# Kernel optimization log

Hardware: AMD Instinct MI355X
Metric: run time of the kernel (lower is better)

The kernel has to match this reference:

```python
import jax, jax.numpy as jnp
import numpy as np

ALPHA = 0.2  # LeakyReLU negative slope
N, IN_DIM, OUT_DIM = 8192, 128, 64


def setup_inputs() -> dict:
    key = jax.random.key(0)
    k1, k2, k3, k4 = jax.random.split(key, 4)
    x = jax.random.normal(k1, (N, IN_DIM), dtype=jnp.float32)
    adj = jax.random.randint(k2, (N, N), 0, 2, dtype=jnp.int32)
    W = jax.random.normal(k3, (IN_DIM, OUT_DIM), dtype=jnp.float32) * 0.1
    a = jax.random.normal(k4, (2 * OUT_DIM, 1), dtype=jnp.float32) * 0.1
    return {"x": x, "adj": adj, "W": W, "a": a}


def reference(x, adj, W, a):
    # h = x @ W : [N, out]
    h = x @ W
    # e_ij = LeakyReLU(a^T [h_i || h_j]) computed as broadcast sum of the
    # two halves of the attention vector (avoids materializing [N,N,2*out]).
    a_src = a[:OUT_DIM, 0]   # [out]
    a_dst = a[OUT_DIM:, 0]   # [out]
    e = (h @ a_src)[:, None] + (h @ a_dst)[None, :]      # [N, N]
    e = jnp.where(e > 0, e, ALPHA * e)                    # LeakyReLU
    # mask non-edges, row-softmax
    e = jnp.where(adj > 0, e, jnp.float32(-9e15))
    attn = jax.nn.softmax(e, axis=-1)                     # [N, N]
    out = attn @ h                                        # [N, out]
    # concat=True -> ELU nonlinearity
    return jax.nn.elu(out)
```

## Files before the change

### kernel.cpp

```cpp
#include <hip/hip_runtime.h>
#include <hip/hip_bf16.h>
#include <cstdint>
#include <cstddef>

#define N_NODES 8192
#define IN_DIM  128
#define OUT_DIM 64
#define LRELU_ALPHA 0.2f
#define S_SLICES 4
#define LOG2E 1.44269504f

using f32x16 = __attribute__((ext_vector_type(16))) float;
using bf16x8 = __attribute__((ext_vector_type(8))) short;

typedef const __attribute__((address_space(1))) int* gas_ptr;
typedef __attribute__((address_space(3))) int* las_ptr;

static __device__ __forceinline__ unsigned short f2bf(float x) {
    union { float f; unsigned u; } v; v.f = x;
    unsigned r = v.u + 0x7FFFu + ((v.u >> 16) & 1u);
    return (unsigned short)(r >> 16);
}

__global__ __launch_bounds__(256) void gat_prep(
    const float* __restrict__ x, const float* __restrict__ W,
    const float* __restrict__ a,
    float* __restrict__ svec, float* __restrict__ dvec,
    unsigned short* __restrict__ hpack)
{
    __shared__ float shA[4][8][64];
    const int tid = threadIdx.x;
    const int w   = tid >> 6;
    const int f   = tid & 63;
    const int i0  = blockIdx.x * 8;

    float acc[8];
#pragma unroll
    for (int r = 0; r < 8; ++r) acc[r] = 0.f;

    const int k0 = w * 32;
#pragma unroll 2
    for (int k = k0; k < k0 + 32; k += 4) {
        const float w0 = W[(k + 0) * OUT_DIM + f];
        const float w1 = W[(k + 1) * OUT_DIM + f];
        const float w2 = W[(k + 2) * OUT_DIM + f];
        const float w3 = W[(k + 3) * OUT_DIM + f];
#pragma unroll
        for (int r = 0; r < 8; ++r) {
            const float4 xv = *reinterpret_cast<const float4*>(
                x + (size_t)(i0 + r) * IN_DIM + k);
            acc[r] = fmaf(xv.x, w0, acc[r]);
            acc[r] = fmaf(xv.y, w1, acc[r]);
            acc[r] = fmaf(xv.z, w2, acc[r]);
            acc[r] = fmaf(xv.w, w3, acc[r]);
        }
    }
#pragma unroll
    for (int r = 0; r < 8; ++r) shA[w][r][f] = acc[r];
    __syncthreads();

    if (w == 0) {
        union { unsigned short us[8]; int4 v; } pk;
#pragma unroll
        for (int r = 0; r < 8; ++r) {
            const float hv = shA[0][r][f] + shA[1][r][f] + shA[2][r][f] + shA[3][r][f];
            pk.us[r] = f2bf(hv);
        }
        const int jb    = i0 >> 4;
        const int jhalf = (i0 >> 3) & 1;
        const int fb    = f >> 5;
        const int lidx  = (f & 31) + 32 * jhalf;
        *reinterpret_cast<int4*>(hpack + ((size_t)(jb * 2 + fb) * 64 + lidx) * 8) = pk.v;
    } else if (w == 1) {
        const float asrc = a[f];
#pragma unroll
        for (int r = 0; r < 8; ++r) {
            const float hv = shA[0][r][f] + shA[1][r][f] + shA[2][r][f] + shA[3][r][f];
            float sv = hv * asrc;
#pragma unroll
            for (int off = 32; off >= 1; off >>= 1) sv += __shfl_xor(sv, off);
            if (f == 0) svec[i0 + r] = sv * LOG2E;
        }
    } else if (w == 2) {
        const float adst = a[OUT_DIM + f];
#pragma unroll
        for (int r = 0; r < 8; ++r) {
            const float hv = shA[0][r][f] + shA[1][r][f] + shA[2][r][f] + shA[3][r][f];
            float dv = hv * adst;
#pragma unroll
            for (int off = 32; off >= 1; off >>= 1) dv += __shfl_xor(dv, off);
            if (f == 0) dvec[i0 + r] = dv * LOG2E;
        }
    }
}

__global__ __launch_bounds__(256, 4) void gat_main(
    const int* __restrict__ adj,
    const float* __restrict__ svec, const float* __restrict__ dvec,
    const unsigned short* __restrict__ hpack,
    float* __restrict__ pO, float* __restrict__ pDen)
{
    union SH {
        int tiles[2][32 * 128];
        struct { float red[4][32][64]; float redden[4][32]; } r;
    };
    __shared__ SH sh;

    const int tid = threadIdx.x;
    const int w   = tid >> 6;
    const int l   = tid & 63;
    const int rb  = blockIdx.x;
    const int sl  = blockIdx.y;
    const int row = l & 31;
    const int kh  = l >> 5;
    const int i0  = rb * 32;
    const int jwin = sl * 2048;

    const float s_i = svec[i0 + row];
    const bf16x8* hp = reinterpret_cast<const bf16x8*>(hpack);

    auto stage = [&](int buf, int ss) {
        const int jt0 = jwin + ss * 128;
#pragma unroll
        for (int q = 0; q < 4; ++q) {
            const int r0   = (w * 4 + q) * 2;
            const int lrow = r0 + (l >> 5);
            const int cp   = l & 31;
            const int cg   = cp ^ (lrow & 7);
            const int* gsrc = adj + (size_t)(i0 + lrow) * N_NODES + jt0 + cg * 4;
            int* ldst = &sh.tiles[buf][r0 * 128];
            __builtin_amdgcn_global_load_lds((gas_ptr)gsrc, (las_ptr)ldst, 16, 0, 0);
        }
    };

    f32x16 acc0, acc1;
#pragma unroll
    for (int r = 0; r < 16; ++r) { acc0[r] = 0.f; acc1[r] = 0.f; }
    float den = 0.f;

    stage(0, 0);
    __syncthreads();

    for (int ss = 0; ss < 16; ++ss) {
        const int buf = ss & 1;
        if (ss + 1 < 16) stage(buf ^ 1, ss + 1);

        const int jt0 = jwin + ss * 128;
#pragma unroll
        for (int st = 0; st < 2; ++st) {
            const int jo = w * 32 + st * 16;
            const int jg = jt0 + jo;
            const int c0 = (jo >> 2) + kh * 2;
            const int4 A0 = *reinterpret_cast<const int4*>(
                &sh.tiles[buf][row * 128 + ((c0    ) ^ (row & 7)) * 4]);
            const int4 A1 = *reinterpret_cast<const int4*>(
                &sh.tiles[buf][row * 128 + ((c0 + 1) ^ (row & 7)) * 4]);
            const int j0 = jg + kh * 8;
            const float4 d0 = *reinterpret_cast<const float4*>(dvec + j0);
            const float4 d1 = *reinterpret_cast<const float4*>(dvec + j0 + 4);
            const int jb = jg >> 4;
            const bf16x8 b0 = hp[(jb * 2 + 0) * 64 + l];
            const bf16x8 b1 = hp[(jb * 2 + 1) * 64 + l];

            const float dd[8] = {d0.x, d0.y, d0.z, d0.w, d1.x, d1.y, d1.z, d1.w};
            const int   ia[8] = {A0.x, A0.y, A0.z, A0.w, A1.x, A1.y, A1.z, A1.w};

            bf16x8 af;
#pragma unroll
            for (int e = 0; e < 8; ++e) {
                float ev = s_i + dd[e];
                ev = fmaxf(ev, LRELU_ALPHA * ev);
                float pv = __builtin_amdgcn_exp2f(ev);
                pv = (ia[e] > 0) ? pv : 0.f;
                union { float f; unsigned u; } pu; pu.f = pv;
                pu.u &= 0xFFFF0000u;
                den += pu.f;
                af[e] = (short)(pu.u >> 16);
            }
            acc0 = __builtin_amdgcn_mfma_f32_32x32x16_bf16(af, b0, acc0, 0, 0, 0);
            acc1 = __builtin_amdgcn_mfma_f32_32x32x16_bf16(af, b1, acc1, 0, 0, 0);
        }
        __syncthreads();
    }

#pragma unroll
    for (int r = 0; r < 16; ++r) {
        const int orow = (r & 3) + 8 * (r >> 2) + 4 * kh;
        sh.r.red[w][orow][row]      = acc0[r];
        sh.r.red[w][orow][32 + row] = acc1[r];
    }
    const float dtot = den + __shfl_xor(den, 32);
    if (l < 32) sh.r.redden[w][l] = dtot;
    __syncthreads();

    float* po = pO + ((size_t)rb * S_SLICES + sl) * 2048;
    const float* rf = &sh.r.red[0][0][0];
    for (int e = tid; e < 2048; e += 256)
        po[e] = rf[e] + rf[2048 + e] + rf[4096 + e] + rf[6144 + e];
    if (tid < 32) {
        pDen[((size_t)rb * S_SLICES + sl) * 32 + tid] =
            sh.r.redden[0][tid] + sh.r.redden[1][tid] +
            sh.r.redden[2][tid] + sh.r.redden[3][tid];
    }
}

__global__ __launch_bounds__(256) void gat_final(
    const float* __restrict__ pO, const float* __restrict__ pDen,
    float* __restrict__ out)
{
    const int idx = blockIdx.x * 256 + threadIdx.x;
    const int i = idx >> 6;
    const int f = idx & 63;
    const int rb = i >> 5;
    const int r  = i & 31;
    const float* po = pO + (size_t)rb * S_SLICES * 2048 + r * 64 + f;
    const float v = po[0] + po[2048] + po[4096] + po[6144];
    const float* pd = pDen + (size_t)rb * S_SLICES * 32 + r;
    const float dsum = pd[0] + pd[32] + pd[64] + pd[96];
    const float o = v / dsum;
    out[idx] = (o > 0.f) ? o : expm1f(o);
}

extern "C" void kernel_launch(void* const* d_in, const int* in_sizes, int n_in,
                              void* d_out, int out_size, void* d_ws, size_t ws_size,
                              hipStream_t stream)
{
    const float* x   = (const float*)d_in[0];
    const int*   adj = (const int*)d_in[1];
    const float* W   = (const float*)d_in[2];
    const float* a   = (const float*)d_in[3];
    float* out = (float*)d_out;

    float* svec = (float*)d_ws;
    float* dvec = svec + N_NODES;
    unsigned short* hpack = (unsigned short*)(dvec + N_NODES);
    float* pO = (float*)(hpack + (size_t)N_NODES * OUT_DIM);
    float* pDen = pO + (size_t)256 * S_SLICES * 2048;

    gat_prep<<<N_NODES / 8, 256, 0, stream>>>(x, W, a, svec, dvec, hpack);
    gat_main<<<dim3(256, S_SLICES), 256, 0, stream>>>(adj, svec, dvec, hpack, pO, pDen);
    gat_final<<<(N_NODES * OUT_DIM) / 256, 256, 0, stream>>>(pO, pDen, out);
}
```

Baseline: 72.13 us.

## Give each wave private adj/h staging with per-wave async pipeline, no block barriers

Each wave now owns a contiguous 512-column slice of the j window. It stages its own 32x16 adj tile plus the packed bf16 h fragments into private LDS double buffers via global_load_lds, and preloads its dvec slice into LDS. Explicit vmcnt/lgkmcnt waits replace the per-iteration __syncthreads, removing block-wide barriers and the direct global loads of h and dvec. The smaller per-step tiles mean more, smaller async loads. The hand-written waitcnt values must match the number of outstanding loads exactly.

```diff
diff --git a/kernel.cpp b/kernel.cpp
--- a/kernel.cpp
+++ b/kernel.cpp
@@ -97,11 +97,14 @@
 __global__ __launch_bounds__(256, 4) void gat_main(
     const int* __restrict__ adj,
     const float* __restrict__ svec, const float* __restrict__ dvec,
-    const unsigned short* __restrict__ hpack,
+    const int* __restrict__ hpk,
     float* __restrict__ pO, float* __restrict__ pDen)
 {
     union SH {
-        int tiles[2][32 * 128];
+        struct {
+            int tiles[4][2][1024];
+            float dvl[2048];
+        } s;
         struct { float red[4][32][64]; float redden[4][32]; } r;
     };
     __shared__ SH sh;
@@ -114,24 +117,38 @@
     const int row = l & 31;
     const int kh  = l >> 5;
     const int i0  = rb * 32;
-    const int jwin = sl * 2048;
+    const int jwv = sl * 2048 + w * 512;
 
     const float s_i = svec[i0 + row];
-    const bf16x8* hp = reinterpret_cast<const bf16x8*>(hpack);
-
-    auto stage = [&](int buf, int ss) {
-        const int jt0 = jwin + ss * 128;
-#pragma unroll
-        for (int q = 0; q < 4; ++q) {
-            const int r0   = (w * 4 + q) * 2;
-            const int lrow = r0 + (l >> 5);
-            const int cp   = l & 31;
-            const int cg   = cp ^ (lrow & 7);
-            const int* gsrc = adj + (size_t)(i0 + lrow) * N_NODES + jt0 + cg * 4;
-            int* ldst = &sh.tiles[buf][r0 * 128];
-            __builtin_amdgcn_global_load_lds((gas_ptr)gsrc, (las_ptr)ldst, 16, 0, 0);
+    const int lrow_a = l >> 2;
+    const int ucol_a = l & 3;
+
+    auto stage = [&](int buf, int t) {
+        const int jt0 = jwv + t * 16;
+        const int jb2 = (jt0 >> 4) * 2;
+#pragma unroll
+        for (int q = 0; q < 2; ++q) {
+            const int r16 = q * 16 + lrow_a;
+            const int up  = ucol_a ^ ((r16 >> 1) & 3);
+            const int* gs = adj + (size_t)(i0 + r16) * N_NODES + jt0 + up * 4;
+            __builtin_amdgcn_global_load_lds((gas_ptr)gs,
+                (las_ptr)&sh.s.tiles[w][buf][q * 256], 16, 0, 0);
+        }
+#pragma unroll
+        for (int q = 0; q < 2; ++q) {
+            const int* gs = hpk + ((size_t)(jb2 + q) * 64 + l) * 4;
+            __builtin_amdgcn_global_load_lds((gas_ptr)gs,
+                (las_ptr)&sh.s.tiles[w][buf][512 + q * 256], 16, 0, 0);
         }
     };
+
+#pragma unroll
+    for (int q = 0; q < 2; ++q) {
+        const int* gs = (const int*)dvec + jwv + q * 256 + l * 4;
+        __builtin_amdgcn_global_load_lds((gas_ptr)gs,
+            (las_ptr)((__attribute__((address_space(3))) int*)&sh.s.dvl[w * 512 + q * 256]),
+            16, 0, 0);
+    }
 
     f32x16 acc0, acc1;
 #pragma unroll
@@ -139,49 +156,52 @@
     float den = 0.f;
 
     stage(0, 0);
+    stage(1, 1);
+
+    const int swz = (row >> 1) & 3;
+    auto body = [&](int t, bool last) {
+        const int buf = t & 1;
+        if (last) asm volatile("s_waitcnt vmcnt(0)" ::: "memory");
+        else      asm volatile("s_waitcnt vmcnt(4)" ::: "memory");
+        __builtin_amdgcn_sched_barrier(0);
+
+        const int* tb = &sh.s.tiles[w][buf][0];
+        const int u0 = (2 * kh)     ^ swz;
+        const int u1 = (2 * kh + 1) ^ swz;
+        const int4 A0 = *reinterpret_cast<const int4*>(&tb[row * 16 + u0 * 4]);
+        const int4 A1 = *reinterpret_cast<const int4*>(&tb[row * 16 + u1 * 4]);
+        const bf16x8 b0 = *reinterpret_cast<const bf16x8*>(&tb[512 + l * 4]);
+        const bf16x8 b1 = *reinterpret_cast<const bf16x8*>(&tb[768 + l * 4]);
+        const int dbase = w * 512 + t * 16 + kh * 8;
+        const float4 d0 = *reinterpret_cast<const float4*>(&sh.s.dvl[dbase]);
+        const float4 d1 = *reinterpret_cast<const float4*>(&sh.s.dvl[dbase + 4]);
+
+        asm volatile("s_waitcnt lgkmcnt(0)" ::: "memory");
+        __builtin_amdgcn_sched_barrier(0);
+        if (t + 2 < 32) stage(buf, t + 2);
+
+        const float dd[8] = {d0.x, d0.y, d0.z, d0.w, d1.x, d1.y, d1.z, d1.w};
+        const int   ia[8] = {A0.x, A0.y, A0.z, A0.w, A1.x, A1.y, A1.z, A1.w};
+        bf16x8 af;
+#pragma unroll
+        for (int e = 0; e < 8; ++e) {
+            float ev = s_i + dd[e];
+            ev = fmaxf(ev, LRELU_ALPHA * ev);
+            float pv = __builtin_amdgcn_exp2f(ev);
+            pv = (ia[e] > 0) ? pv : 0.f;
+            union { float f; unsigned u; } pu; pu.f = pv;
+            pu.u &= 0xFFFF0000u;
+            den += pu.f;
+            af[e] = (short)(pu.u >> 16);
+        }
+        acc0 = __builtin_amdgcn_mfma_f32_32x32x16_bf16(af, b0, acc0, 0, 0, 0);
+        acc1 = __builtin_amdgcn_mfma_f32_32x32x16_bf16(af, b1, acc1, 0, 0, 0);
+    };
+
+    for (int t = 0; t < 31; ++t) body(t, false);
+    body(31, true);
+
     __syncthreads();
-
-    for (int ss = 0; ss < 16; ++ss) {
-        const int buf = ss & 1;
-        if (ss + 1 < 16) stage(buf ^ 1, ss + 1);
-
-        const int jt0 = jwin + ss * 128;
-#pragma unroll
-        for (int st = 0; st < 2; ++st) {
-            const int jo = w * 32 + st * 16;
-            const int jg = jt0 + jo;
-            const int c0 = (jo >> 2) + kh * 2;
-            const int4 A0 = *reinterpret_cast<const int4*>(
-                &sh.tiles[buf][row * 128 + ((c0    ) ^ (row & 7)) * 4]);
-            const int4 A1 = *reinterpret_cast<const int4*>(
-                &sh.tiles[buf][row * 128 + ((c0 + 1) ^ (row & 7)) * 4]);
-            const int j0 = jg + kh * 8;
-            const float4 d0 = *reinterpret_cast<const float4*>(dvec + j0);
-            const float4 d1 = *reinterpret_cast<const float4*>(dvec + j0 + 4);
-            const int jb = jg >> 4;
-            const bf16x8 b0 = hp[(jb * 2 + 0) * 64 + l];
-            const bf16x8 b1 = hp[(jb * 2 + 1) * 64 + l];
-
-            const float dd[8] = {d0.x, d0.y, d0.z, d0.w, d1.x, d1.y, d1.z, d1.w};
-            const int   ia[8] = {A0.x, A0.y, A0.z, A0.w, A1.x, A1.y, A1.z, A1.w};
-
-            bf16x8 af;
-#pragma unroll
-            for (int e = 0; e < 8; ++e) {
-                float ev = s_i + dd[e];
-                ev = fmaxf(ev, LRELU_ALPHA * ev);
-                float pv = __builtin_amdgcn_exp2f(ev);
-                pv = (ia[e] > 0) ? pv : 0.f;
-                union { float f; unsigned u; } pu; pu.f = pv;
-                pu.u &= 0xFFFF0000u;
-                den += pu.f;
-                af[e] = (short)(pu.u >> 16);
-            }
-            acc0 = __builtin_amdgcn_mfma_f32_32x32x16_bf16(af, b0, acc0, 0, 0, 0);
-            acc1 = __builtin_amdgcn_mfma_f32_32x32x16_bf16(af, b1, acc1, 0, 0, 0);
-        }
-        __syncthreads();
-    }
 
 #pragma unroll
     for (int r = 0; r < 16; ++r) {
@@ -238,6 +258,7 @@
     float* pDen = pO + (size_t)256 * S_SLICES * 2048;
 
     gat_prep<<<N_NODES / 8, 256, 0, stream>>>(x, W, a, svec, dvec, hpack);
-    gat_main<<<dim3(256, S_SLICES), 256, 0, stream>>>(adj, svec, dvec, hpack, pO, pDen);
+    gat_main<<<dim3(256, S_SLICES), 256, 0, stream>>>(adj, svec, dvec,
+                                                      (const int*)hpack, pO, pDen);
     gat_final<<<(N_NODES * OUT_DIM) / 256, 256, 0, stream>>>(pO, pDen, out);
 }
```

After: 86.71 us. +20.2%, slower.

## Prefetch adjacency two stages ahead with explicit waitcnt and split barriers

Applied to the files above, without the earlier changes.

Restructures the main loop so adjacency tiles are staged two iterations ahead into the double buffer, with explicit vmcnt waits and raw s_barrier instead of __syncthreads. The hpack and dvec loads for both sub-steps are issued before the wait, so global latency overlaps the LDS tile arrival. The next stage is issued into the just-consumed buffer after the LDS reads drain. Correctness depends on the hand-counted vmcnt(12) matching the compiler's order of outstanding loads.

```diff
diff --git a/kernel.cpp b/kernel.cpp
--- a/kernel.cpp
+++ b/kernel.cpp
@@ -117,6 +117,7 @@
     const int jwin = sl * 2048;
 
     const float s_i = svec[i0 + row];
+    asm volatile("" :: "v"(s_i));
     const bf16x8* hp = reinterpret_cast<const bf16x8*>(hpack);
 
     auto stage = [&](int buf, int ss) {
@@ -139,49 +140,75 @@
     float den = 0.f;
 
     stage(0, 0);
+    stage(1, 1);
+
+    const int swz = row & 7;
+    for (int s = 0; s < 16; ++s) {
+        const int buf = s & 1;
+        const int jt0 = jwin + s * 128;
+        const int jg  = jt0 + w * 32;
+        const int jb  = jg >> 4;
+
+        const bf16x8 b00 = hp[(jb * 2 + 0) * 64 + l];
+        const bf16x8 b01 = hp[(jb * 2 + 1) * 64 + l];
+        const bf16x8 b10 = hp[(jb * 2 + 2) * 64 + l];
+        const bf16x8 b11 = hp[(jb * 2 + 3) * 64 + l];
+        const int j0 = jg + kh * 8;
+        const float4 dA0 = *reinterpret_cast<const float4*>(dvec + j0);
+        const float4 dA1 = *reinterpret_cast<const float4*>(dvec + j0 + 4);
+        const float4 dB0 = *reinterpret_cast<const float4*>(dvec + j0 + 16);
+        const float4 dB1 = *reinterpret_cast<const float4*>(dvec + j0 + 20);
+
+        asm volatile("s_waitcnt vmcnt(12)" ::: "memory");
+        __builtin_amdgcn_s_barrier();
+
+        const int* tb = &sh.tiles[buf][0];
+        const int c00 = w * 8 + kh * 2;
+        const int c10 = w * 8 + 4 + kh * 2;
+        const int4 A00 = *reinterpret_cast<const int4*>(&tb[row * 128 + ((c00    ) ^ swz) * 4]);
+        const int4 A01 = *reinterpret_cast<const int4*>(&tb[row * 128 + ((c00 + 1) ^ swz) * 4]);
+        const int4 A10 = *reinterpret_cast<const int4*>(&tb[row * 128 + ((c10    ) ^ swz) * 4]);
+        const int4 A11 = *reinterpret_cast<const int4*>(&tb[row * 128 + ((c10 + 1) ^ swz) * 4]);
+        asm volatile("s_waitcnt lgkmcnt(0)" ::: "memory");
+        __builtin_amdgcn_s_barrier();
+
+        if (s + 2 < 16) stage(buf, s + 2);
+
+        const float dd0[8] = {dA0.x, dA0.y, dA0.z, dA0.w, dA1.x, dA1.y, dA1.z, dA1.w};
+        const int   ia0[8] = {A00.x, A00.y, A00.z, A00.w, A01.x, A01.y, A01.z, A01.w};
+        const float dd1[8] = {dB0.x, dB0.y, dB0.z, dB0.w, dB1.x, dB1.y, dB1.z, dB1.w};
+        const int   ia1[8] = {A10.x, A10.y, A10.z, A10.w, A11.x, A11.y, A11.z, A11.w};
+
+        bf16x8 af0, af1;
+#pragma unroll
+        for (int e = 0; e < 8; ++e) {
+            float ev = s_i + dd0[e];
+            ev = fmaxf(ev, LRELU_ALPHA * ev);
+            float pv = __builtin_amdgcn_exp2f(ev);
+            pv = (ia0[e] > 0) ? pv : 0.f;
+            union { float f; unsigned u; } pu; pu.f = pv;
+            pu.u &= 0xFFFF0000u;
+            den += pu.f;
+            af0[e] = (short)(pu.u >> 16);
+        }
+#pragma unroll
+        for (int e = 0; e < 8; ++e) {
+            float ev = s_i + dd1[e];
+            ev = fmaxf(ev, LRELU_ALPHA * ev);
+            float pv = __builtin_amdgcn_exp2f(ev);
+            pv = (ia1[e] > 0) ? pv : 0.f;
+            union { float f; unsigned u; } pu; pu.f = pv;
+            pu.u &= 0xFFFF0000u;
+            den += pu.f;
+            af1[e] = (short)(pu.u >> 16);
+        }
+        acc0 = __builtin_amdgcn_mfma_f32_32x32x16_bf16(af0, b00, acc0, 0, 0, 0);
+        acc1 = __builtin_amdgcn_mfma_f32_32x32x16_bf16(af0, b01, acc1, 0, 0, 0);
+        acc0 = __builtin_amdgcn_mfma_f32_32x32x16_bf16(af1, b10, acc0, 0, 0, 0);
+        acc1 = __builtin_amdgcn_mfma_f32_32x32x16_bf16(af1, b11, acc1, 0, 0, 0);
+    }
+
     __syncthreads();
-
-    for (int ss = 0; ss < 16; ++ss) {
-        const int buf = ss & 1;
-        if (ss + 1 < 16) stage(buf ^ 1, ss + 1);
-
-        const int jt0 = jwin + ss * 128;
-#pragma unroll
-        for (int st = 0; st < 2; ++st) {
-            const int jo = w * 32 + st * 16;
-            const int jg = jt0 + jo;
-            const int c0 = (jo >> 2) + kh * 2;
-            const int4 A0 = *reinterpret_cast<const int4*>(
-                &sh.tiles[buf][row * 128 + ((c0    ) ^ (row & 7)) * 4]);
-            const int4 A1 = *reinterpret_cast<const int4*>(
-                &sh.tiles[buf][row * 128 + ((c0 + 1) ^ (row & 7)) * 4]);
-            const int j0 = jg + kh * 8;
-            const float4 d0 = *reinterpret_cast<const float4*>(dvec + j0);
-            const float4 d1 = *reinterpret_cast<const float4*>(dvec + j0 + 4);
-            const int jb = jg >> 4;
-            const bf16x8 b0 = hp[(jb * 2 + 0) * 64 + l];
-            const bf16x8 b1 = hp[(jb * 2 + 1) * 64 + l];
-
-            const float dd[8] = {d0.x, d0.y, d0.z, d0.w, d1.x, d1.y, d1.z, d1.w};
-            const int   ia[8] = {A0.x, A0.y, A0.z, A0.w, A1.x, A1.y, A1.z, A1.w};
-
-            bf16x8 af;
-#pragma unroll
-            for (int e = 0; e < 8; ++e) {
-                float ev = s_i + dd[e];
-                ev = fmaxf(ev, LRELU_ALPHA * ev);
-                float pv = __builtin_amdgcn_exp2f(ev);
-                pv = (ia[e] > 0) ? pv : 0.f;
-                union { float f; unsigned u; } pu; pu.f = pv;
-                pu.u &= 0xFFFF0000u;
-                den += pu.f;
-                af[e] = (short)(pu.u >> 16);
-            }
-            acc0 = __builtin_amdgcn_mfma_f32_32x32x16_bf16(af, b0, acc0, 0, 0, 0);
-            acc1 = __builtin_amdgcn_mfma_f32_32x32x16_bf16(af, b1, acc1, 0, 0, 0);
-        }
-        __syncthreads();
-    }
 
 #pragma unroll
     for (int r = 0; r < 16; ++r) {
```

Measured after the change: 70.71 us. 2.0% less time.
